# Optimization experiments

Hardware: AMD Instinct MI355X
Metric: run time of the kernel (lower is better)

## Reference

```python
import math
import jax, jax.numpy as jnp
import numpy as np

DIM = 256; DEPTH = 5; FANOUT = 10; VOCAB = 257
B = 16; T = 2048
NEXP = 8; HID = 512; TOPK = 2; TEMP = 1.0; HEADS = 2
CAPACITY = math.ceil(B * TOPK / NEXP * 1.1)  # capacity-based dispatch, =5
LAYER_SIZES = [FANOUT ** l for l in range(DEPTH)]  # [1,10,100,1000,10000]


def setup_inputs() -> dict:
    key = jax.random.key(0)
    ks = iter(jax.random.split(key, 64))
    def p(shape, scale=0.02):
        return jax.random.normal(next(ks), shape, jnp.float32) * scale
    inp = {
        'tokens': jax.random.randint(next(ks), (B, T), 0, VOCAB),
        'embed': p((VOCAB, DIM)),
        'pin_w': p((DIM, DIM)), 'pin_b': jnp.zeros(DIM, jnp.float32),
        'pch_w': p((DIM, DIM)), 'pch_b': jnp.zeros(DIM, jnp.float32),
        'depth_bias': p((DEPTH, DIM)),
        'q_w': p((DIM, DIM)), 'q_b': jnp.zeros(DIM, jnp.float32),
        'k_w': p((DIM, DIM)), 'k_b': jnp.zeros(DIM, jnp.float32),
        'v_w': p((DIM, DIM)), 'v_b': jnp.zeros(DIM, jnp.float32),
        'o_w': p((DIM, DIM)), 'o_b': jnp.zeros(DIM, jnp.float32),
        'level_gate': jnp.zeros(DEPTH, jnp.float32),
        'depth_gate': jnp.zeros((DEPTH, DIM), jnp.float32),
        'in_proj_w': p((DIM, 3 * DIM)), 'in_proj_b': jnp.zeros(3 * DIM, jnp.float32),
        'out_proj_w': p((DIM, DIM)), 'out_proj_b': jnp.zeros(DIM, jnp.float32),
        'ln_g': jnp.ones(DIM, jnp.float32), 'ln_b': jnp.zeros(DIM, jnp.float32),
        'ic_gate': jnp.zeros(1, jnp.float32),
        'gate_w': p((DIM, NEXP)), 'gate_b': jnp.zeros(NEXP, jnp.float32),
        'ew1': p((NEXP, DIM, HID)), 'eb1': jnp.zeros((NEXP, HID), jnp.float32),
        'ew2': p((NEXP, HID, DIM)), 'eb2': jnp.zeros((NEXP, DIM), jnp.float32),
        'hw1': p((DIM, DIM)), 'hb1': jnp.zeros(DIM, jnp.float32),
        'hw2': p((DIM, VOCAB)), 'hb2': jnp.zeros(VOCAB, jnp.float32),
    }
    return inp


def _fractal(context, pin_w, pin_b, pch_w, pch_b, depth_bias, q_w, q_b, k_w, k_b,
             v_w, v_b, o_w, o_b, level_gate, depth_gate,
             in_proj_w, in_proj_b, out_proj_w, out_proj_b, ln_g, ln_b, ic_gate):
    Bc = context.shape[0]
    base = context @ pin_w + pin_b                       # [B,D]
    y_next = None
    level_means = [None] * DEPTH
    inv_sqrt_d = 1.0 / math.sqrt(DIM)
    for l in reversed(range(DEPTH)):
        n = LAYER_SIZES[l]
        if l == DEPTH - 1:
            child_agg = jnp.zeros((Bc, n, DIM), context.dtype)
        else:
            yg = y_next.reshape(Bc, n, FANOUT, DIM)      # children grouped per parent
            q = (base + depth_bias[l]) @ q_w + q_b       # [B,D], shared across nodes
            k = yg @ k_w + k_b
            v = yg @ v_w + v_b
            att = jax.nn.softmax(jnp.einsum('bd,bnfd->bnf', q, k) * inv_sqrt_d, axis=-1)
            child_agg = jax.nn.sigmoid(depth_gate[l]) * jnp.einsum('bnf,bnfd->bnd', att, v)
        gate = jax.nn.sigmoid(level_gate[l])
        upd = (base[:, None, :] + depth_bias[l][None, None, :] + child_agg @ pch_w + pch_b) * gate
        y = jax.nn.relu(upd) @ o_w + o_b                 # [B,n,D]
        level_means[l] = y.mean(axis=1)
        y_next = y
    root = y_next[:, 0, :]                               # n==1 at level 0
    # interconnect: MHA over per-level means [B,DEPTH,D]
    z = jnp.stack(level_means, axis=1)
    qkv = z @ in_proj_w + in_proj_b
    qh, kh, vh = jnp.split(qkv, 3, axis=-1)
    hd = DIM // HEADS
    def to_heads(t):
        return t.reshape(Bc, DEPTH, HEADS, hd).transpose(0, 2, 1, 3)
    qh, kh, vh = to_heads(qh), to_heads(kh), to_heads(vh)
    aw = jax.nn.softmax(jnp.einsum('bhqd,bhkd->bhqk', qh, kh) / math.sqrt(hd), axis=-1)
    z2 = jnp.einsum('bhqk,bhkd->bhqd', aw, vh).transpose(0, 2, 1, 3).reshape(Bc, DEPTH, DIM)
    z2 = z2 @ out_proj_w + out_proj_b
    zs = z + z2
    mu = zs.mean(-1, keepdims=True)
    var = ((zs - mu) ** 2).mean(-1, keepdims=True)
    zn = (zs - mu) / jnp.sqrt(var + 1e-5) * ln_g + ln_b
    return root + jax.nn.sigmoid(ic_gate) * zn[:, 0, :]


def _moe(ctx, gate_w, gate_b, ew1, eb1, ew2, eb2):
    scaled = (ctx @ gate_w + gate_b) / TEMP
    top_vals, top_idx = jax.lax.top_k(scaled, TOPK)      # [B,K]
    gs = jax.nn.softmax(top_vals, axis=-1)               # [B,K], strictly > 0
    out = jnp.zeros_like(ctx)
    for e in range(NEXP):                                # fixed small expert loop
        sflat = jnp.where(top_idx == e, gs, -1.0).reshape(-1)   # [B*K]
        vals, pos = jax.lax.top_k(sflat, CAPACITY)       # capacity-limited dispatch
        w = jnp.where(vals > 0.0, vals, 0.0)             # drop unassigned/overflow
        tok = pos // TOPK
        xin = ctx[tok]                                   # [cap,D]
        eo = jax.nn.relu(xin @ ew1[e] + eb1[e]) @ ew2[e] + eb2[e]
        out = out.at[tok].add(eo * w[:, None])
    return out


def reference(tokens, embed, pin_w, pin_b, pch_w, pch_b, depth_bias,
              q_w, q_b, k_w, k_b, v_w, v_b, o_w, o_b, level_gate, depth_gate,
              in_proj_w, in_proj_b, out_proj_w, out_proj_b, ln_g, ln_b, ic_gate,
              gate_w, gate_b, ew1, eb1, ew2, eb2, hw1, hb1, hw2, hb2):
    x = embed[tokens]                                    # [B,T,D]
    context = x.mean(axis=1)                             # [B,D]
    root = _fractal(context, pin_w, pin_b, pch_w, pch_b, depth_bias, q_w, q_b,
                    k_w, k_b, v_w, v_b, o_w, o_b, level_gate, depth_gate,
                    in_proj_w, in_proj_b, out_proj_w, out_proj_b, ln_g, ln_b, ic_gate)
    root = root + _moe(root, gate_w, gate_b, ew1, eb1, ew2, eb2)
    h = x + root[:, None, :]                             # per-token logits from context + token emb
    logits = jax.nn.relu(h @ hw1 + hb1) @ hw2 + hb2      # [B,T,V]
    return logits
```

## Files before the change

kernel.cpp:

```cpp
#include <hip/hip_runtime.h>
#include <hip/hip_bf16.h>
#include <math.h>

#define DIM    256
#define DEPTH  5
#define FANOUT 10
#define VOCAB  257
#define BB     16
#define TT     2048
#define NEXP   8
#define HID    512
#define TOPK   2
#define CAP    5
#define TSTR   260

__device__ __forceinline__ float sigm(float x) { return 1.f / (1.f + expf(-x)); }

__device__ __forceinline__ float dotcol64(const float* sv, const float* __restrict__ W,
                                          int col, int k0, int stride) {
  float acc = 0.f;
#pragma unroll 8
  for (int i = 0; i < 64; ++i) {
    int k = k0 + i;
    acc = fmaf(sv[k], W[(size_t)k * stride + col], acc);
  }
  return acc;
}

__global__ void __launch_bounds__(1024) k_fractal(
    const int* __restrict__ tokens, const float* __restrict__ embed,
    const float* __restrict__ pin_w, const float* __restrict__ pin_b,
    const float* __restrict__ pch_w, const float* __restrict__ pch_b,
    const float* __restrict__ depth_bias,
    const float* __restrict__ v_w, const float* __restrict__ v_b,
    const float* __restrict__ o_w, const float* __restrict__ o_b,
    const float* __restrict__ level_gate, const float* __restrict__ depth_gate,
    const float* __restrict__ in_proj_w, const float* __restrict__ in_proj_b,
    const float* __restrict__ out_proj_w, const float* __restrict__ out_proj_b,
    const float* __restrict__ ln_g, const float* __restrict__ ln_b,
    const float* __restrict__ ic_gate,
    float* __restrict__ rootA) {
  int b = blockIdx.x;
  int tid = threadIdx.x;
  int d = tid & 255;
  int ks = tid >> 8;
  int k0 = ks * 64;
  __shared__ int cnt[VOCAB];
  __shared__ float sv[DIM];
  __shared__ float basev[DIM];
  __shared__ float ym[DEPTH][DIM];
  __shared__ float q0v[DIM], kh[DEPTH][DIM], vh[DEPTH][DIM];
  __shared__ float red4[4][DIM];
  __shared__ float red11[4][11][DIM];
  __shared__ float zsv[DIM];
  __shared__ float aw[16];
  __shared__ float redl[8];

  for (int i = tid; i < VOCAB; i += 1024) cnt[i] = 0;
  __syncthreads();
  for (int t = tid; t < TT; t += 1024) atomicAdd(&cnt[tokens[b * TT + t]], 1);
  __syncthreads();
  {
    float acc = 0.f;
#pragma unroll
    for (int h = 0; h < 2; ++h) {
      int vb = ks * 64 + h * 32;
      float ev[32], cv[32];
#pragma unroll
      for (int i = 0; i < 32; ++i) ev[i] = embed[(size_t)(vb + i) * DIM + d];
#pragma unroll
      for (int i = 0; i < 32; ++i) cv[i] = (float)cnt[vb + i];
#pragma unroll
      for (int i = 0; i < 32; ++i) acc = fmaf(cv[i], ev[i], acc);
    }
    if (ks == 0) acc = fmaf((float)cnt[256], embed[(size_t)256 * DIM + d], acc);
    red4[ks][d] = acc;
  }
  __syncthreads();
  if (ks == 0)
    sv[d] = (red4[0][d] + red4[1][d] + red4[2][d] + red4[3][d]) * (1.0f / (float)TT);
  __syncthreads();

  red4[ks][d] = dotcol64(sv, pin_w, d, k0, DIM);
  __syncthreads();
  if (ks == 0) {
    float base = red4[0][d] + red4[1][d] + red4[2][d] + red4[3][d] + pin_b[d];
    basev[d] = base;
    float u = (base + depth_bias[4 * DIM + d] + pch_b[d]) * sigm(level_gate[4]);
    sv[d] = fmaxf(u, 0.f);
  }
  __syncthreads();
  red4[ks][d] = dotcol64(sv, o_w, d, k0, DIM);
  __syncthreads();
  if (ks == 0) {
    float y = red4[0][d] + red4[1][d] + red4[2][d] + red4[3][d] + o_b[d];
    ym[4][d] = y;
    sv[d] = y;
  }
  __syncthreads();
  for (int l = 3; l >= 0; --l) {
    red4[ks][d] = dotcol64(sv, v_w, d, k0, DIM);
    __syncthreads();
    if (ks == 0) {
      float vv = red4[0][d] + red4[1][d] + red4[2][d] + red4[3][d] + v_b[d];
      sv[d] = sigm(depth_gate[l * DIM + d]) * vv;
    }
    __syncthreads();
    red4[ks][d] = dotcol64(sv, pch_w, d, k0, DIM);
    __syncthreads();
    if (ks == 0) {
      float t = red4[0][d] + red4[1][d] + red4[2][d] + red4[3][d] + pch_b[d];
      float u = (basev[d] + depth_bias[l * DIM + d] + t) * sigm(level_gate[l]);
      sv[d] = fmaxf(u, 0.f);
    }
    __syncthreads();
    red4[ks][d] = dotcol64(sv, o_w, d, k0, DIM);
    __syncthreads();
    if (ks == 0) {
      float y = red4[0][d] + red4[1][d] + red4[2][d] + red4[3][d] + o_b[d];
      ym[l][d] = y;
      sv[d] = y;
    }
    __syncthreads();
  }
  {
    float aq = 0.f;
    float ak0 = 0.f, ak1 = 0.f, ak2 = 0.f, ak3 = 0.f, ak4 = 0.f;
    float av0 = 0.f, av1 = 0.f, av2 = 0.f, av3 = 0.f, av4 = 0.f;
#pragma unroll
    for (int h = 0; h < 8; ++h) {
      int kb = k0 + h * 8;
      float wq[8], wk[8], wv8[8];
#pragma unroll
      for (int i = 0; i < 8; ++i) {
        const float* wrow = in_proj_w + (size_t)(kb + i) * 768;
        wq[i] = wrow[d]; wk[i] = wrow[256 + d]; wv8[i] = wrow[512 + d];
      }
#pragma unroll
      for (int i = 0; i < 8; ++i) {
        float z0 = ym[0][kb + i];
        aq  = fmaf(z0, wq[i], aq);
        ak0 = fmaf(z0, wk[i], ak0);
        av0 = fmaf(z0, wv8[i], av0);
        float z1 = ym[1][kb + i];
        ak1 = fmaf(z1, wk[i], ak1);
        av1 = fmaf(z1, wv8[i], av1);
        float z2 = ym[2][kb + i];
        ak2 = fmaf(z2, wk[i], ak2);
        av2 = fmaf(z2, wv8[i], av2);
        float z3 = ym[3][kb + i];
        ak3 = fmaf(z3, wk[i], ak3);
        av3 = fmaf(z3, wv8[i], av3);
        float z4 = ym[4][kb + i];
        ak4 = fmaf(z4, wk[i], ak4);
        av4 = fmaf(z4, wv8[i], av4);
      }
    }
    red11[ks][0][d] = ak0; red11[ks][1][d] = ak1; red11[ks][2][d] = ak2;
    red11[ks][3][d] = ak3; red11[ks][4][d] = ak4;
    red11[ks][5][d] = av0; red11[ks][6][d] = av1; red11[ks][7][d] = av2;
    red11[ks][8][d] = av3; red11[ks][9][d] = av4;
    red11[ks][10][d] = aq;
  }
  __syncthreads();
  for (int idx = tid; idx < 11 * DIM; idx += 1024) {
    int c = idx >> 8, dd = idx & 255;
    float sum = red11[0][c][dd] + red11[1][c][dd] + red11[2][c][dd] + red11[3][c][dd];
    if (c < 5)       kh[c][dd]     = sum + in_proj_b[256 + dd];
    else if (c < 10) vh[c - 5][dd] = sum + in_proj_b[512 + dd];
    else             q0v[dd]       = sum + in_proj_b[dd];
  }
  __syncthreads();
  if (tid < 10) {
    int h = tid / 5, l = tid - h * 5;
    float s = 0.f;
    for (int j = 0; j < 128; ++j) s = fmaf(q0v[h * 128 + j], kh[l][h * 128 + j], s);
    aw[tid] = s * 0.08838834764831845f;
  }
  __syncthreads();
  if (tid < 2) {
    float m = aw[tid * 5];
    for (int l = 1; l < 5; ++l) m = fmaxf(m, aw[tid * 5 + l]);
    float e[5], ssum = 0.f;
    for (int l = 0; l < 5; ++l) { e[l] = expf(aw[tid * 5 + l] - m); ssum += e[l]; }
    for (int l = 0; l < 5; ++l) aw[tid * 5 + l] = e[l] / ssum;
  }
  __syncthreads();
  if (ks == 0) {
    int h = d >> 7;
    float z2 = 0.f;
    for (int l = 0; l < 5; ++l) z2 = fmaf(aw[h * 5 + l], vh[l][d], z2);
    sv[d] = z2;
  }
  __syncthreads();
  red4[ks][d] = dotcol64(sv, out_proj_w, d, k0, DIM);
  __syncthreads();
  if (ks == 0) {
    float z2p = red4[0][d] + red4[1][d] + red4[2][d] + red4[3][d] + out_proj_b[d];
    zsv[d] = ym[0][d] + z2p;
  }
  __syncthreads();
  float zs = 0.f, df = 0.f, mu = 0.f;
  if (tid < 256) {
    zs = zsv[tid];
    float v = zs;
    for (int o = 32; o > 0; o >>= 1) v += __shfl_down(v, o, 64);
    if ((tid & 63) == 0) redl[tid >> 6] = v;
  }
  __syncthreads();
  if (tid < 256) {
    mu = (redl[0] + redl[1] + redl[2] + redl[3]) * (1.f / 256.f);
    df = zs - mu;
  }
  __syncthreads();
  if (tid < 256) {
    float v = df * df;
    for (int o = 32; o > 0; o >>= 1) v += __shfl_down(v, o, 64);
    if ((tid & 63) == 0) redl[tid >> 6] = v;
  }
  __syncthreads();
  if (tid < 256) {
    float var = (redl[0] + redl[1] + redl[2] + redl[3]) * (1.f / 256.f);
    float zn = df / sqrtf(var + 1e-5f) * ln_g[tid] + ln_b[tid];
    rootA[b * DIM + tid] = ym[0][tid] + sigm(ic_gate[0]) * zn;
  }
}

__global__ void __launch_bounds__(1024) k_gate(const float* __restrict__ rootA,
                                               const float* __restrict__ gate_w,
                                               const float* __restrict__ gate_b,
                                               int* __restrict__ etok,
                                               float* __restrict__ ewt,
                                               float* __restrict__ root2) {
  __shared__ float red[BB * NEXP][9];
  __shared__ float sc[BB * NEXP];
  __shared__ float gs[BB * TOPK];
  __shared__ int gidx[BB * TOPK];
  int tid = threadIdx.x;
  int be = tid >> 3, ks = tid & 7;
  int b = be >> 3, e = be & 7;
  {
    float acc = 0.f;
#pragma unroll 8
    for (int i = 0; i < 32; ++i) {
      int k = ks * 32 + i;
      acc = fmaf(rootA[b * DIM + k], gate_w[k * NEXP + e], acc);
    }
    red[be][ks] = acc;
  }
  for (int i = tid; i < BB * DIM; i += 1024) root2[i] = rootA[i];
  __syncthreads();
  if (tid < BB * NEXP) {
    float s = gate_b[tid & 7];
#pragma unroll
    for (int g = 0; g < 8; ++g) s += red[tid][g];
    sc[tid] = s;
  }
  __syncthreads();
  if (tid < BB) {
    int bb = tid;
    int i0 = 0; float v0 = sc[bb * 8 + 0];
    for (int ee = 1; ee < 8; ++ee) { float v = sc[bb * 8 + ee]; if (v > v0) { v0 = v; i0 = ee; } }
    int i1 = -1; float v1 = -1e30f;
    for (int ee = 0; ee < 8; ++ee) {
      if (ee == i0) continue;
      float v = sc[bb * 8 + ee];
      if (v > v1) { v1 = v; i1 = ee; }
    }
    float e1 = expf(v1 - v0);
    float s = 1.f + e1;
    gs[bb * 2 + 0] = 1.f / s;  gidx[bb * 2 + 0] = i0;
    gs[bb * 2 + 1] = e1 / s;   gidx[bb * 2 + 1] = i1;
  }
  __syncthreads();
  if (tid < NEXP) {
    int ee = tid;
    float vals[32];
    bool used[32];
    for (int i = 0; i < 32; ++i) { vals[i] = (gidx[i] == ee) ? gs[i] : -1.0f; used[i] = false; }
    for (int s = 0; s < CAP; ++s) {
      int bi = -1; float bv = -1e30f;
      for (int i = 0; i < 32; ++i) {
        if (used[i]) continue;
        if (vals[i] > bv) { bv = vals[i]; bi = i; }
      }
      used[bi] = true;
      etok[ee * CAP + s] = bi >> 1;
      ewt[ee * CAP + s] = bv > 0.f ? bv : 0.f;
    }
  }
}

__global__ void __launch_bounds__(256) k_expert1(
    const float* __restrict__ rootA,
    const float* __restrict__ ew1, const float* __restrict__ eb1,
    const int* __restrict__ etok,
    float* __restrict__ hid_ws) {
  int bx = blockIdx.x;
  int e = bx >> 3, jt = bx & 7, j0 = jt * 64;
  int tid = threadIdx.x, w = tid >> 6, lane = tid & 63;
  __shared__ float xin[CAP][DIM];
  __shared__ float red[CAP][4][64];
  __shared__ int stok[CAP];
  if (tid < CAP) stok[tid] = etok[e * CAP + tid];
  __syncthreads();
  for (int idx = tid; idx < CAP * DIM; idx += 256) {
    int s = idx >> 8, k = idx & 255;
    xin[s][k] = rootA[stok[s] * DIM + k];
  }
  __syncthreads();
  float a0 = 0.f, a1 = 0.f, a2 = 0.f, a3 = 0.f, a4 = 0.f;
  const float* W = ew1 + (size_t)e * DIM * HID + j0 + lane;
  int kbase = w * 64;
#pragma unroll
  for (int h = 0; h < 8; ++h) {
    float wv[8];
#pragma unroll
    for (int i = 0; i < 8; ++i) wv[i] = W[(size_t)(kbase + h * 8 + i) * HID];
#pragma unroll
    for (int i = 0; i < 8; ++i) {
      int k = kbase + h * 8 + i;
      a0 = fmaf(xin[0][k], wv[i], a0);
      a1 = fmaf(xin[1][k], wv[i], a1);
      a2 = fmaf(xin[2][k], wv[i], a2);
      a3 = fmaf(xin[3][k], wv[i], a3);
      a4 = fmaf(xin[4][k], wv[i], a4);
    }
  }
  red[0][w][lane] = a0; red[1][w][lane] = a1; red[2][w][lane] = a2;
  red[3][w][lane] = a3; red[4][w][lane] = a4;
  __syncthreads();
  for (int idx = tid; idx < CAP * 64; idx += 256) {
    int s = idx >> 6, j = idx & 63;
    float sum = red[s][0][j] + red[s][1][j] + red[s][2][j] + red[s][3][j]
              + eb1[e * HID + j0 + j];
    hid_ws[((size_t)(e * CAP + s)) * HID + j0 + j] = fmaxf(sum, 0.f);
  }
}

__global__ void __launch_bounds__(256) k_expert2(
    const float* __restrict__ hid_ws,
    const float* __restrict__ ew2, const float* __restrict__ eb2,
    const float* __restrict__ ewt, const int* __restrict__ etok,
    float* __restrict__ root2) {
  int bx = blockIdx.x;
  int e = bx >> 3, dt = bx & 7, d0 = dt * 32;
  int tid = threadIdx.x, seg = tid >> 5, c = tid & 31;
  __shared__ float hv[CAP][HID];
  __shared__ float red[CAP][8][32];
  for (int idx = tid; idx < CAP * HID; idx += 256) {
    int s = idx >> 9, k = idx & 511;
    hv[s][k] = hid_ws[((size_t)(e * CAP + s)) * HID + k];
  }
  __syncthreads();
  float a0 = 0.f, a1 = 0.f, a2 = 0.f, a3 = 0.f, a4 = 0.f;
  const float* W = ew2 + (size_t)e * HID * DIM + d0 + c;
  int kbase = seg * 64;
#pragma unroll
  for (int h = 0; h < 8; ++h) {
    float wv[8];
#pragma unroll
    for (int i = 0; i < 8; ++i) wv[i] = W[(size_t)(kbase + h * 8 + i) * DIM];
#pragma unroll
    for (int i = 0; i < 8; ++i) {
      int k = kbase + h * 8 + i;
      a0 = fmaf(hv[0][k], wv[i], a0);
      a1 = fmaf(hv[1][k], wv[i], a1);
      a2 = fmaf(hv[2][k], wv[i], a2);
      a3 = fmaf(hv[3][k], wv[i], a3);
      a4 = fmaf(hv[4][k], wv[i], a4);
    }
  }
  red[0][seg][c] = a0; red[1][seg][c] = a1; red[2][seg][c] = a2;
  red[3][seg][c] = a3; red[4][seg][c] = a4;
  __syncthreads();
  if (tid < CAP * 32) {
    int s = tid >> 5, cc = tid & 31;
    float sum = 0.f;
#pragma unroll
    for (int g = 0; g < 8; ++g) sum += red[s][g][cc];
    sum += eb2[e * DIM + d0 + cc];
    float w = ewt[e * CAP + s];
    if (w > 0.f)
      atomicAdd(&root2[etok[e * CAP + s] * DIM + d0 + cc], sum * w);
  }
}

__global__ void __launch_bounds__(256) k_table(
    const float* __restrict__ embed, const float* __restrict__ root2,
    const float* __restrict__ hw1, const float* __restrict__ hb1,
    const float* __restrict__ hw2, const float* __restrict__ hb2,
    float* __restrict__ table) {
  int tok = blockIdx.x, r0 = blockIdx.y * 4;
  int c = threadIdx.x;
  __shared__ float hrow[4][DIM];
  __shared__ float hid[4][DIM];
  __shared__ float tailred[4][17];
  {
    float ev = embed[(size_t)tok * DIM + c];
#pragma unroll
    for (int j = 0; j < 4; ++j) hrow[j][c] = ev + root2[(size_t)(r0 + j) * DIM + c];
  }
  __syncthreads();
  {
    float a0 = hb1[c], a1 = a0, a2 = a0, a3 = a0;
    for (int kb = 0; kb < DIM; kb += 8) {
      float wv[8];
#pragma unroll
      for (int i = 0; i < 8; ++i) wv[i] = hw1[(size_t)(kb + i) * DIM + c];
#pragma unroll
      for (int i = 0; i < 8; ++i) {
        int k = kb + i;
        a0 = fmaf(hrow[0][k], wv[i], a0);
        a1 = fmaf(hrow[1][k], wv[i], a1);
        a2 = fmaf(hrow[2][k], wv[i], a2);
        a3 = fmaf(hrow[3][k], wv[i], a3);
      }
    }
    hid[0][c] = fmaxf(a0, 0.f); hid[1][c] = fmaxf(a1, 0.f);
    hid[2][c] = fmaxf(a2, 0.f); hid[3][c] = fmaxf(a3, 0.f);
  }
  __syncthreads();
  {
    float a0 = hb2[c], a1 = a0, a2 = a0, a3 = a0;
    for (int kb = 0; kb < DIM; kb += 8) {
      float wv[8];
#pragma unroll
      for (int i = 0; i < 8; ++i) wv[i] = hw2[(size_t)(kb + i) * VOCAB + c];
#pragma unroll
      for (int i = 0; i < 8; ++i) {
        int k = kb + i;
        a0 = fmaf(hid[0][k], wv[i], a0);
        a1 = fmaf(hid[1][k], wv[i], a1);
        a2 = fmaf(hid[2][k], wv[i], a2);
        a3 = fmaf(hid[3][k], wv[i], a3);
      }
    }
    table[((size_t)((r0 + 0) * VOCAB + tok)) * TSTR + c] = a0;
    table[((size_t)((r0 + 1) * VOCAB + tok)) * TSTR + c] = a1;
    table[((size_t)((r0 + 2) * VOCAB + tok)) * TSTR + c] = a2;
    table[((size_t)((r0 + 3) * VOCAB + tok)) * TSTR + c] = a3;
  }
  if (c < 64) {
    int r = c >> 4, seg = c & 15;
    float sum = 0.f;
#pragma unroll 4
    for (int i = 0; i < 16; ++i) {
      int k = seg * 16 + i;
      sum = fmaf(hid[r][k], hw2[(size_t)k * VOCAB + 256], sum);
    }
    tailred[r][seg] = sum;
  }
  __syncthreads();
  if (c < 4) {
    float a = hb2[256];
#pragma unroll
    for (int s = 0; s < 16; ++s) a += tailred[c][s];
    table[((size_t)((r0 + c) * VOCAB + tok)) * TSTR + 256] = a;
  }
}

__global__ void __launch_bounds__(1024) k_scatter(const int* __restrict__ tokens,
                                                  const float* __restrict__ table,
                                                  float* __restrict__ out) {
  int f = blockIdx.x * 1024 + threadIdx.x;
  int row = (int)((unsigned)f / 257u);
  int c = f - row * 257;
  int b = row >> 11;
  int tok = tokens[row];
  out[f] = table[((size_t)(b * VOCAB + tok)) * TSTR + c];
}

extern "C" void kernel_launch(void* const* d_in, const int* in_sizes, int n_in,
                              void* d_out, int out_size, void* d_ws, size_t ws_size,
                              hipStream_t stream) {
  (void)in_sizes; (void)n_in; (void)out_size; (void)ws_size;
  const int*   tokens     = (const int*)d_in[0];
  const float* embed      = (const float*)d_in[1];
  const float* pin_w      = (const float*)d_in[2];
  const float* pin_b      = (const float*)d_in[3];
  const float* pch_w      = (const float*)d_in[4];
  const float* pch_b      = (const float*)d_in[5];
  const float* depth_bias = (const float*)d_in[6];
  const float* v_w        = (const float*)d_in[11];
  const float* v_b        = (const float*)d_in[12];
  const float* o_w        = (const float*)d_in[13];
  const float* o_b        = (const float*)d_in[14];
  const float* level_gate = (const float*)d_in[15];
  const float* depth_gate = (const float*)d_in[16];
  const float* in_proj_w  = (const float*)d_in[17];
  const float* in_proj_b  = (const float*)d_in[18];
  const float* out_proj_w = (const float*)d_in[19];
  const float* out_proj_b = (const float*)d_in[20];
  const float* ln_g       = (const float*)d_in[21];
  const float* ln_b       = (const float*)d_in[22];
  const float* ic_gate    = (const float*)d_in[23];
  const float* gate_w     = (const float*)d_in[24];
  const float* gate_b     = (const float*)d_in[25];
  const float* ew1        = (const float*)d_in[26];
  const float* eb1        = (const float*)d_in[27];
  const float* ew2        = (const float*)d_in[28];
  const float* eb2        = (const float*)d_in[29];
  const float* hw1        = (const float*)d_in[30];
  const float* hb1        = (const float*)d_in[31];
  const float* hw2        = (const float*)d_in[32];
  const float* hb2        = (const float*)d_in[33];
  float* out = (float*)d_out;

  float* ws      = (float*)d_ws;
  float* rootA   = ws + 4096;
  float* root2   = ws + 8192;
  int*   etok    = (int*)(ws + 22528);
  float* ewt     = ws + 22576;
  float* table   = ws + 22656;
  float* hid_ws  = table;

  k_fractal<<<BB, 1024, 0, stream>>>(tokens, embed, pin_w, pin_b, pch_w, pch_b,
                                     depth_bias, v_w, v_b, o_w, o_b, level_gate,
                                     depth_gate, in_proj_w, in_proj_b, out_proj_w,
                                     out_proj_b, ln_g, ln_b, ic_gate, rootA);
  k_gate<<<1, 1024, 0, stream>>>(rootA, gate_w, gate_b, etok, ewt, root2);
  k_expert1<<<NEXP * 8, 256, 0, stream>>>(rootA, ew1, eb1, etok, hid_ws);
  k_expert2<<<NEXP * 8, 256, 0, stream>>>(hid_ws, ew2, eb2, ewt, etok, root2);
  k_table<<<dim3(VOCAB, 4), 256, 0, stream>>>(embed, root2, hw1, hb1, hw2, hb2, table);
  k_scatter<<<(BB * TT * VOCAB) / 1024, 1024, 0, stream>>>(tokens, table, out);
}
```

Baseline: 270.4 us.

## Vectorize fractal matvecs with float4 loads and 16-way K split

Replaces the per-column scalar dot product (4-way K split) with a matvec in which each thread loads float4 columns across 16 rows, using a 16-way K split whose partials are reduced through shared memory reused from red11. The embedding count-weighted sum is restructured the same way. The q·k attention scores are now computed by warps with shuffle reductions instead of 10 serial threads, and the MoE capacity selection uses a bitmask instead of local arrays. The goal is wider, better-coalesced global loads and more parallelism in the serial latency-bound chain, at the cost of a larger 16-term shared-memory reduction per step.

```diff
diff --git a/kernel.cpp b/kernel.cpp
--- a/kernel.cpp
+++ b/kernel.cpp
@@ -16,15 +16,30 @@
 
 __device__ __forceinline__ float sigm(float x) { return 1.f / (1.f + expf(-x)); }
 
-__device__ __forceinline__ float dotcol64(const float* sv, const float* __restrict__ W,
-                                          int col, int k0, int stride) {
-  float acc = 0.f;
-#pragma unroll 8
-  for (int i = 0; i < 64; ++i) {
-    int k = k0 + i;
-    acc = fmaf(sv[k], W[(size_t)k * stride + col], acc);
-  }
-  return acc;
+__device__ __forceinline__ void mv16(const float* sv, const float* __restrict__ W,
+                                     int kseg, int cq, float red[16][DIM]) {
+  const float* Wp = W + (size_t)kseg * 16 * DIM + cq * 4;
+  float4 wv[16];
+#pragma unroll
+  for (int i = 0; i < 16; ++i)
+    wv[i] = *(const float4*)(Wp + (size_t)i * DIM);
+  float4 acc = {0.f, 0.f, 0.f, 0.f};
+#pragma unroll
+  for (int i = 0; i < 16; ++i) {
+    float s = sv[kseg * 16 + i];
+    acc.x = fmaf(s, wv[i].x, acc.x);
+    acc.y = fmaf(s, wv[i].y, acc.y);
+    acc.z = fmaf(s, wv[i].z, acc.z);
+    acc.w = fmaf(s, wv[i].w, acc.w);
+  }
+  *(float4*)&red[kseg][cq * 4] = acc;
+}
+
+__device__ __forceinline__ float sum16(const float red[16][DIM], int d) {
+  float s = 0.f;
+#pragma unroll
+  for (int g = 0; g < 16; ++g) s += red[g][d];
+  return s;
 }
 
 __global__ void __launch_bounds__(1024) k_fractal(
@@ -45,79 +60,84 @@
   int d = tid & 255;
   int ks = tid >> 8;
   int k0 = ks * 64;
+  int kseg = tid >> 6;
+  int cq = tid & 63;
   __shared__ int cnt[VOCAB];
   __shared__ float sv[DIM];
   __shared__ float basev[DIM];
   __shared__ float ym[DEPTH][DIM];
   __shared__ float q0v[DIM], kh[DEPTH][DIM], vh[DEPTH][DIM];
-  __shared__ float red4[4][DIM];
   __shared__ float red11[4][11][DIM];
   __shared__ float zsv[DIM];
   __shared__ float aw[16];
   __shared__ float redl[8];
+  float (*red16)[DIM] = reinterpret_cast<float(*)[DIM]>(&red11[0][0][0]);
 
   for (int i = tid; i < VOCAB; i += 1024) cnt[i] = 0;
   __syncthreads();
   for (int t = tid; t < TT; t += 1024) atomicAdd(&cnt[tokens[b * TT + t]], 1);
   __syncthreads();
   {
-    float acc = 0.f;
-#pragma unroll
-    for (int h = 0; h < 2; ++h) {
-      int vb = ks * 64 + h * 32;
-      float ev[32], cv[32];
-#pragma unroll
-      for (int i = 0; i < 32; ++i) ev[i] = embed[(size_t)(vb + i) * DIM + d];
-#pragma unroll
-      for (int i = 0; i < 32; ++i) cv[i] = (float)cnt[vb + i];
-#pragma unroll
-      for (int i = 0; i < 32; ++i) acc = fmaf(cv[i], ev[i], acc);
-    }
-    if (ks == 0) acc = fmaf((float)cnt[256], embed[(size_t)256 * DIM + d], acc);
-    red4[ks][d] = acc;
-  }
-  __syncthreads();
-  if (ks == 0)
-    sv[d] = (red4[0][d] + red4[1][d] + red4[2][d] + red4[3][d]) * (1.0f / (float)TT);
-  __syncthreads();
-
-  red4[ks][d] = dotcol64(sv, pin_w, d, k0, DIM);
+    const float* Ep = embed + (size_t)kseg * 16 * DIM + cq * 4;
+    float4 ev[16];
+#pragma unroll
+    for (int i = 0; i < 16; ++i) ev[i] = *(const float4*)(Ep + (size_t)i * DIM);
+    float4 acc = {0.f, 0.f, 0.f, 0.f};
+#pragma unroll
+    for (int i = 0; i < 16; ++i) {
+      float cv = (float)cnt[kseg * 16 + i];
+      acc.x = fmaf(cv, ev[i].x, acc.x);
+      acc.y = fmaf(cv, ev[i].y, acc.y);
+      acc.z = fmaf(cv, ev[i].z, acc.z);
+      acc.w = fmaf(cv, ev[i].w, acc.w);
+    }
+    *(float4*)&red16[kseg][cq * 4] = acc;
+  }
   __syncthreads();
   if (ks == 0) {
-    float base = red4[0][d] + red4[1][d] + red4[2][d] + red4[3][d] + pin_b[d];
+    float s = sum16(red16, d);
+    s = fmaf((float)cnt[256], embed[(size_t)256 * DIM + d], s);
+    sv[d] = s * (1.0f / (float)TT);
+  }
+  __syncthreads();
+
+  mv16(sv, pin_w, kseg, cq, red16);
+  __syncthreads();
+  if (ks == 0) {
+    float base = sum16(red16, d) + pin_b[d];
     basev[d] = base;
     float u = (base + depth_bias[4 * DIM + d] + pch_b[d]) * sigm(level_gate[4]);
     sv[d] = fmaxf(u, 0.f);
   }
   __syncthreads();
-  red4[ks][d] = dotcol64(sv, o_w, d, k0, DIM);
+  mv16(sv, o_w, kseg, cq, red16);
   __syncthreads();
   if (ks == 0) {
-    float y = red4[0][d] + red4[1][d] + red4[2][d] + red4[3][d] + o_b[d];
+    float y = sum16(red16, d) + o_b[d];
     ym[4][d] = y;
     sv[d] = y;
   }
   __syncthreads();
   for (int l = 3; l >= 0; --l) {
-    red4[ks][d] = dotcol64(sv, v_w, d, k0, DIM);
+    mv16(sv, v_w, kseg, cq, red16);
     __syncthreads();
     if (ks == 0) {
-      float vv = red4[0][d] + red4[1][d] + red4[2][d] + red4[3][d] + v_b[d];
+      float vv = sum16(red16, d) + v_b[d];
       sv[d] = sigm(depth_gate[l * DIM + d]) * vv;
     }
     __syncthreads();
-    red4[ks][d] = dotcol64(sv, pch_w, d, k0, DIM);
+    mv16(sv, pch_w, kseg, cq, red16);
     __syncthreads();
     if (ks == 0) {
-      float t = red4[0][d] + red4[1][d] + red4[2][d] + red4[3][d] + pch_b[d];
+      float t = sum16(red16, d) + pch_b[d];
       float u = (basev[d] + depth_bias[l * DIM + d] + t) * sigm(level_gate[l]);
       sv[d] = fmaxf(u, 0.f);
     }
     __syncthreads();
-    red4[ks][d] = dotcol64(sv, o_w, d, k0, DIM);
+    mv16(sv, o_w, kseg, cq, red16);
     __syncthreads();
     if (ks == 0) {
-      float y = red4[0][d] + red4[1][d] + red4[2][d] + red4[3][d] + o_b[d];
+      float y = sum16(red16, d) + o_b[d];
       ym[l][d] = y;
       sv[d] = y;
     }
@@ -128,16 +148,16 @@
     float ak0 = 0.f, ak1 = 0.f, ak2 = 0.f, ak3 = 0.f, ak4 = 0.f;
     float av0 = 0.f, av1 = 0.f, av2 = 0.f, av3 = 0.f, av4 = 0.f;
 #pragma unroll
-    for (int h = 0; h < 8; ++h) {
-      int kb = k0 + h * 8;
-      float wq[8], wk[8], wv8[8];
-#pragma unroll
-      for (int i = 0; i < 8; ++i) {
+    for (int h = 0; h < 4; ++h) {
+      int kb = k0 + h * 16;
+      float wq[16], wk[16], wv8[16];
+#pragma unroll
+      for (int i = 0; i < 16; ++i) {
         const float* wrow = in_proj_w + (size_t)(kb + i) * 768;
         wq[i] = wrow[d]; wk[i] = wrow[256 + d]; wv8[i] = wrow[512 + d];
       }
 #pragma unroll
-      for (int i = 0; i < 8; ++i) {
+      for (int i = 0; i < 16; ++i) {
         float z0 = ym[0][kb + i];
         aq  = fmaf(z0, wq[i], aq);
         ak0 = fmaf(z0, wk[i], ak0);
@@ -171,11 +191,16 @@
     else             q0v[dd]       = sum + in_proj_b[dd];
   }
   __syncthreads();
-  if (tid < 10) {
-    int h = tid / 5, l = tid - h * 5;
-    float s = 0.f;
-    for (int j = 0; j < 128; ++j) s = fmaf(q0v[h * 128 + j], kh[l][h * 128 + j], s);
-    aw[tid] = s * 0.08838834764831845f;
+  {
+    int wid = tid >> 6;
+    if (wid < 10) {
+      int h = wid / 5, l = wid - h * 5;
+      int lane = tid & 63;
+      float s = q0v[h * 128 + lane] * kh[l][h * 128 + lane];
+      s = fmaf(q0v[h * 128 + 64 + lane], kh[l][h * 128 + 64 + lane], s);
+      for (int o = 32; o > 0; o >>= 1) s += __shfl_down(s, o, 64);
+      if (lane == 0) aw[wid] = s * 0.08838834764831845f;
+    }
   }
   __syncthreads();
   if (tid < 2) {
@@ -193,10 +218,10 @@
     sv[d] = z2;
   }
   __syncthreads();
-  red4[ks][d] = dotcol64(sv, out_proj_w, d, k0, DIM);
+  mv16(sv, out_proj_w, kseg, cq, red16);
   __syncthreads();
   if (ks == 0) {
-    float z2p = red4[0][d] + red4[1][d] + red4[2][d] + red4[3][d] + out_proj_b[d];
+    float z2p = sum16(red16, d) + out_proj_b[d];
     zsv[d] = ym[0][d] + z2p;
   }
   __syncthreads();
@@ -275,16 +300,15 @@
   __syncthreads();
   if (tid < NEXP) {
     int ee = tid;
-    float vals[32];
-    bool used[32];
-    for (int i = 0; i < 32; ++i) { vals[i] = (gidx[i] == ee) ? gs[i] : -1.0f; used[i] = false; }
+    unsigned used = 0u;
     for (int s = 0; s < CAP; ++s) {
-      int bi = -1; float bv = -1e30f;
+      int bi = 0; float bv = -1e30f;
       for (int i = 0; i < 32; ++i) {
-        if (used[i]) continue;
-        if (vals[i] > bv) { bv = vals[i]; bi = i; }
+        if (used & (1u << i)) continue;
+        float v = (gidx[i] == ee) ? gs[i] : -1.0f;
+        if (v > bv) { bv = v; bi = i; }
       }
-      used[bi] = true;
+      used |= (1u << bi);
       etok[ee * CAP + s] = bi >> 1;
       ewt[ee * CAP + s] = bv > 0.f ? bv : 0.f;
     }
```

Measured after the change: 336.7 us. 1.25x slower.
